# Kernel optimization log

Measured on AMD Instinct MI355X. Metric: run time of the kernel, lower is better.

## Reference

```python
import jax, jax.numpy as jnp
import numpy as np

N, NQ, NV, NE = 4, 256, 512, 256


def setup_inputs() -> dict:
    key = jax.random.key(0)
    ks = jax.random.split(key, 6)
    scale = 1.0 / np.sqrt(NE)
    return {
        "query": jax.random.normal(ks[0], (N, NQ, NE), dtype=jnp.float32),
        "context": jax.random.normal(ks[1], (N, NV, NE), dtype=jnp.float32),
        "memory": jax.random.normal(ks[2], (N, NV, NE), dtype=jnp.float32),
        "w_logit": jax.random.normal(ks[3], (NE,), dtype=jnp.float32) * scale,
        "b_logit": jnp.zeros((), dtype=jnp.float32),
        "temp": jnp.ones((), dtype=jnp.float32),
        "w_reduce": jax.random.normal(ks[4], (NE, NE), dtype=jnp.float32) * scale,
        "b_reduce": jnp.zeros((NE,), dtype=jnp.float32),
    }


def reference(query, context, memory, w_logit, b_logit, temp, w_reduce, b_reduce):
    # Additive (Bahdanau) attention, single-head branch of the torch module.
    # qc: [N, nQ, nV, nE] -- the large broadcast-add + tanh intermediate
    qc = jnp.tanh(query[:, :, None, :] + context[:, None, :, :])
    # fc_logit: Linear(nE -> 1), squeeze last dim -> [N, nQ, nV]
    logits = jnp.einsum("nqve,e->nqv", qc, w_logit) + b_logit
    probs = jax.nn.softmax(logits / temp, axis=2)
    # bmm(probs, memory) -> [N, nQ, nE], then leaky_relu (torch default slope 0.01)
    heads = jax.nn.leaky_relu(jnp.einsum("nqv,nve->nqe", probs, memory), negative_slope=0.01)
    # fc_reduceheads: Linear(nE -> nE), torch semantics y = x @ W.T + b
    return heads @ w_reduce.T + b_reduce
```

## Files before the change

kernel.cpp:

```cpp
#include <hip/hip_runtime.h>
#include <math.h>

#define N_B   4
#define NQ_   256
#define NV_   512
#define NE_   256

#define QSCALE 2.8853900817779268f

__device__ __forceinline__ float wave_reduce_sum(float v) {
#pragma unroll
    for (int m = 32; m > 0; m >>= 1) v += __shfl_xor(v, m, 64);
    return v;
}

__global__ __launch_bounds__(256) void prep_kernel(const float* __restrict__ C,
                                                   const float* __restrict__ W,
                                                   float* __restrict__ CT,
                                                   float* __restrict__ WT) {
    __shared__ float tile[64][65];
    const int b = blockIdx.x;
    const int col = threadIdx.x & 63, row4 = threadIdx.x >> 6;
    if (b < 128) {
        const int n  = b >> 5;
        const int e0 = ((b >> 3) & 3) * 64;
        const int v0 = (b & 7) * 64;
        const float* src = C + ((size_t)n * NV_ + v0) * NE_ + e0;
#pragma unroll
        for (int r = 0; r < 16; ++r) {
            const int vl = row4 + r * 4;
            tile[vl][col] = src[(size_t)vl * NE_ + col] * QSCALE;
        }
        __syncthreads();
        float* dst = CT + ((size_t)n * NE_ + e0) * NV_ + v0;
#pragma unroll
        for (int r = 0; r < 16; ++r) {
            const int el = row4 + r * 4;
            dst[(size_t)el * NV_ + col] = tile[col][el];
        }
    } else {
        const int bb = b - 128;
        const int r0 = (bb >> 2) * 64, c0 = (bb & 3) * 64;
        const float* src = W + (size_t)r0 * NE_ + c0;
#pragma unroll
        for (int r = 0; r < 16; ++r) {
            const int rl = row4 + r * 4;
            tile[rl][col] = src[(size_t)rl * NE_ + col];
        }
        __syncthreads();
        float* dst = WT + (size_t)c0 * NE_ + r0;
#pragma unroll
        for (int r = 0; r < 16; ++r) {
            const int cl = row4 + r * 4;
            dst[(size_t)cl * NE_ + col] = tile[col][cl];
        }
    }
}

#define QTA 4
__global__ __launch_bounds__(256, 8) void logits_kernel(
    const float* __restrict__ Q,
    const float* __restrict__ CT,
    const float* __restrict__ WL,
    float* __restrict__ S)
{
    const int n  = blockIdx.z;
    const int q0 = blockIdx.y * QTA;
    const int v0 = blockIdx.x * 64;
    const int tid = threadIdx.x;
    const int wv = tid >> 6, ln = tid & 63;

    __shared__ __align__(16) float s_q[NE_][QTA];
    __shared__ float s_w[NE_];
    __shared__ float s_part[4][QTA][64];

    {
        const int e = tid;
        s_w[e] = WL[e];
#pragma unroll
        for (int j = 0; j < QTA; ++j)
            s_q[e][j] = Q[((size_t)n * NQ_ + q0 + j) * NE_ + e] * QSCALE;
    }
    __syncthreads();

    const float* ct = CT + (size_t)n * NE_ * NV_ + v0 + ln;
    float acc0 = 0.f, acc1 = 0.f, acc2 = 0.f, acc3 = 0.f;
    const int e0 = wv * 64;
#pragma unroll 4
    for (int e = e0; e < e0 + 64; ++e) {
        const float c = ct[(size_t)e * NV_];
        const float4 q4 = *(const float4*)s_q[e];
        const float w = s_w[e];
        acc0 = fmaf(w, __builtin_amdgcn_rcpf(1.0f + __builtin_amdgcn_exp2f(c + q4.x)), acc0);
        acc1 = fmaf(w, __builtin_amdgcn_rcpf(1.0f + __builtin_amdgcn_exp2f(c + q4.y)), acc1);
        acc2 = fmaf(w, __builtin_amdgcn_rcpf(1.0f + __builtin_amdgcn_exp2f(c + q4.z)), acc2);
        acc3 = fmaf(w, __builtin_amdgcn_rcpf(1.0f + __builtin_amdgcn_exp2f(c + q4.w)), acc3);
    }
    s_part[wv][0][ln] = acc0;
    s_part[wv][1][ln] = acc1;
    s_part[wv][2][ln] = acc2;
    s_part[wv][3][ln] = acc3;
    __syncthreads();

    {
        const int j = tid >> 6, l = tid & 63;
        const float s = s_part[0][j][l] + s_part[1][j][l]
                      + s_part[2][j][l] + s_part[3][j][l];
        S[((size_t)n * NQ_ + q0 + j) * NV_ + v0 + l] = s;
    }
}

#define QTB 4
#define NWB 8
__global__ __launch_bounds__(512) void attn_out(
    const float* __restrict__ S,
    const float* __restrict__ M,
    const float* __restrict__ TEMP,
    const float* __restrict__ WRT,
    const float* __restrict__ BR,
    float* __restrict__ OUT)
{
    const int n  = blockIdx.y;
    const int q0 = blockIdx.x * QTB;
    const int tid = threadIdx.x;
    const int wv = tid >> 6, ln = tid & 63;

    __shared__ __align__(16) float s_prob[QTB][NV_];
    __shared__ __align__(16) float s_part[NWB][QTB][NE_];
    __shared__ __align__(16) float s_heads[QTB][NE_];

    if (wv < QTB) {
        const float scale = -2.0f / TEMP[0];
        const float* srow = S + ((size_t)n * NQ_ + q0 + wv) * NV_;
        float l[NV_ / 64];
        float mx = -1e30f;
#pragma unroll
        for (int k = 0; k < NV_ / 64; ++k) {
            l[k] = srow[ln + 64 * k] * scale;
            mx = fmaxf(mx, l[k]);
        }
#pragma unroll
        for (int m = 32; m > 0; m >>= 1) mx = fmaxf(mx, __shfl_xor(mx, m, 64));
        float sum = 0.0f;
#pragma unroll
        for (int k = 0; k < NV_ / 64; ++k) {
            l[k] = __expf(l[k] - mx);
            sum += l[k];
        }
        sum = wave_reduce_sum(sum);
        const float inv = 1.0f / sum;
#pragma unroll
        for (int k = 0; k < NV_ / 64; ++k) s_prob[wv][ln + 64 * k] = l[k] * inv;
    }
    __syncthreads();

    {
        const float4* M4 = (const float4*)(M + (size_t)n * NV_ * NE_);
        float4 h[QTB];
#pragma unroll
        for (int t = 0; t < QTB; ++t) h[t] = make_float4(0.f, 0.f, 0.f, 0.f);
        const int v0 = wv * (NV_ / NWB);
#pragma unroll 2
        for (int v = v0; v < v0 + NV_ / NWB; ++v) {
            const float4 m = M4[v * (NE_ / 4) + ln];
#pragma unroll
            for (int t = 0; t < QTB; ++t) {
                const float p = s_prob[t][v];
                h[t].x = fmaf(p, m.x, h[t].x);
                h[t].y = fmaf(p, m.y, h[t].y);
                h[t].z = fmaf(p, m.z, h[t].z);
                h[t].w = fmaf(p, m.w, h[t].w);
            }
        }
#pragma unroll
        for (int t = 0; t < QTB; ++t) ((float4*)s_part[wv][t])[ln] = h[t];
    }
    __syncthreads();

#pragma unroll
    for (int i = tid; i < QTB * NE_; i += 512) {
        const int t = i >> 8, e = i & (NE_ - 1);
        float s = 0.0f;
#pragma unroll
        for (int w = 0; w < NWB; ++w) s += s_part[w][t][e];
        s_heads[t][e] = (s > 0.0f) ? s : 0.01f * s;
    }
    __syncthreads();

    {
        const int t0 = (tid >> 8) * 2;
        const int ep = tid & 255;
        const float* w = WRT + ep;
        float a0 = 0.f, a1 = 0.f;
#pragma unroll 8
        for (int e = 0; e < NE_; ++e) {
            const float wv_ = w[(size_t)e * NE_];
            a0 = fmaf(s_heads[t0][e], wv_, a0);
            a1 = fmaf(s_heads[t0 + 1][e], wv_, a1);
        }
        const float b = BR[ep];
        OUT[((size_t)n * NQ_ + q0 + t0) * NE_ + ep]     = a0 + b;
        OUT[((size_t)n * NQ_ + q0 + t0 + 1) * NE_ + ep] = a1 + b;
    }
}

extern "C" void kernel_launch(void* const* d_in, const int* in_sizes, int n_in,
                              void* d_out, int out_size, void* d_ws, size_t ws_size,
                              hipStream_t stream) {
    const float* Q  = (const float*)d_in[0];
    const float* C  = (const float*)d_in[1];
    const float* M  = (const float*)d_in[2];
    const float* WL = (const float*)d_in[3];
    const float* T  = (const float*)d_in[5];
    const float* WR = (const float*)d_in[6];
    const float* BR = (const float*)d_in[7];
    float* OUT = (float*)d_out;

    float* CT  = (float*)d_ws;
    float* WRT = CT + (size_t)N_B * NE_ * NV_;
    float* S   = WRT + (size_t)NE_ * NE_;

    prep_kernel<<<dim3(128 + 16), 256, 0, stream>>>(C, WR, CT, WRT);

    dim3 ga(NV_ / 64, NQ_ / QTA, N_B);
    logits_kernel<<<ga, 256, 0, stream>>>(Q, CT, WL, S);

    dim3 gb(NQ_ / QTB, N_B);
    attn_out<<<gb, 512, 0, stream>>>(S, M, T, WRT, BR, OUT);
}
```

Before: 122.6 us.

## Factor exp of query plus context and pair terms to share one reciprocal

Context and query are pre-exponentiated, so exp2(c+q) becomes a product and the inner loop runs with no transcendental calls. Pairs of e terms are merged into one fraction (w0/a + w1/b = (w1*a + w0*b)/(a*b)), which halves the number of reciprocals. The aim is to offload the transcendental unit in the logits kernel, which is its bottleneck. In exchange, exponentiating separately can overflow or underflow for large inputs (exp2 of about 2.885*x) and the product a*b can overflow, so accuracy suffers at extreme values.

```diff
diff --git a/kernel.cpp b/kernel.cpp
--- a/kernel.cpp
+++ b/kernel.cpp
@@ -16,7 +16,7 @@
 
 __global__ __launch_bounds__(256) void prep_kernel(const float* __restrict__ C,
                                                    const float* __restrict__ W,
-                                                   float* __restrict__ CT,
+                                                   float* __restrict__ EC,
                                                    float* __restrict__ WT) {
     __shared__ float tile[64][65];
     const int b = blockIdx.x;
@@ -29,10 +29,10 @@
 #pragma unroll
         for (int r = 0; r < 16; ++r) {
             const int vl = row4 + r * 4;
-            tile[vl][col] = src[(size_t)vl * NE_ + col] * QSCALE;
+            tile[vl][col] = __builtin_amdgcn_exp2f(src[(size_t)vl * NE_ + col] * QSCALE);
         }
         __syncthreads();
-        float* dst = CT + ((size_t)n * NE_ + e0) * NV_ + v0;
+        float* dst = EC + ((size_t)n * NE_ + e0) * NV_ + v0;
 #pragma unroll
         for (int r = 0; r < 16; ++r) {
             const int el = row4 + r * 4;
@@ -60,7 +60,7 @@
 #define QTA 4
 __global__ __launch_bounds__(256, 8) void logits_kernel(
     const float* __restrict__ Q,
-    const float* __restrict__ CT,
+    const float* __restrict__ EC,
     const float* __restrict__ WL,
     float* __restrict__ S)
 {
@@ -79,22 +79,45 @@
         s_w[e] = WL[e];
 #pragma unroll
         for (int j = 0; j < QTA; ++j)
-            s_q[e][j] = Q[((size_t)n * NQ_ + q0 + j) * NE_ + e] * QSCALE;
-    }
-    __syncthreads();
-
-    const float* ct = CT + (size_t)n * NE_ * NV_ + v0 + ln;
+            s_q[e][j] = __builtin_amdgcn_exp2f(
+                Q[((size_t)n * NQ_ + q0 + j) * NE_ + e] * QSCALE);
+    }
+    __syncthreads();
+
+    const float* ec = EC + (size_t)n * NE_ * NV_ + v0 + ln;
     float acc0 = 0.f, acc1 = 0.f, acc2 = 0.f, acc3 = 0.f;
     const int e0 = wv * 64;
 #pragma unroll 4
-    for (int e = e0; e < e0 + 64; ++e) {
-        const float c = ct[(size_t)e * NV_];
-        const float4 q4 = *(const float4*)s_q[e];
-        const float w = s_w[e];
-        acc0 = fmaf(w, __builtin_amdgcn_rcpf(1.0f + __builtin_amdgcn_exp2f(c + q4.x)), acc0);
-        acc1 = fmaf(w, __builtin_amdgcn_rcpf(1.0f + __builtin_amdgcn_exp2f(c + q4.y)), acc1);
-        acc2 = fmaf(w, __builtin_amdgcn_rcpf(1.0f + __builtin_amdgcn_exp2f(c + q4.z)), acc2);
-        acc3 = fmaf(w, __builtin_amdgcn_rcpf(1.0f + __builtin_amdgcn_exp2f(c + q4.w)), acc3);
+    for (int e = e0; e < e0 + 64; e += 2) {
+        const float c0 = ec[(size_t)e * NV_];
+        const float c1 = ec[(size_t)(e + 1) * NV_];
+        const float4 qa = *(const float4*)s_q[e];
+        const float4 qb = *(const float4*)s_q[e + 1];
+        const float w0 = s_w[e], w1 = s_w[e + 1];
+        {
+            const float a = fmaf(c0, qa.x, 1.0f);
+            const float b = fmaf(c1, qb.x, 1.0f);
+            const float num = fmaf(w1, a, w0 * b);
+            acc0 = fmaf(num, __builtin_amdgcn_rcpf(a * b), acc0);
+        }
+        {
+            const float a = fmaf(c0, qa.y, 1.0f);
+            const float b = fmaf(c1, qb.y, 1.0f);
+            const float num = fmaf(w1, a, w0 * b);
+            acc1 = fmaf(num, __builtin_amdgcn_rcpf(a * b), acc1);
+        }
+        {
+            const float a = fmaf(c0, qa.z, 1.0f);
+            const float b = fmaf(c1, qb.z, 1.0f);
+            const float num = fmaf(w1, a, w0 * b);
+            acc2 = fmaf(num, __builtin_amdgcn_rcpf(a * b), acc2);
+        }
+        {
+            const float a = fmaf(c0, qa.w, 1.0f);
+            const float b = fmaf(c1, qb.w, 1.0f);
+            const float num = fmaf(w1, a, w0 * b);
+            acc3 = fmaf(num, __builtin_amdgcn_rcpf(a * b), acc3);
+        }
     }
     s_part[wv][0][ln] = acc0;
     s_part[wv][1][ln] = acc1;
@@ -216,14 +239,14 @@
     const float* BR = (const float*)d_in[7];
     float* OUT = (float*)d_out;
 
-    float* CT  = (float*)d_ws;
-    float* WRT = CT + (size_t)N_B * NE_ * NV_;
+    float* EC  = (float*)d_ws;
+    float* WRT = EC + (size_t)N_B * NE_ * NV_;
     float* S   = WRT + (size_t)NE_ * NE_;
 
-    prep_kernel<<<dim3(128 + 16), 256, 0, stream>>>(C, WR, CT, WRT);
+    prep_kernel<<<dim3(144), 256, 0, stream>>>(C, WR, EC, WRT);
 
     dim3 ga(NV_ / 64, NQ_ / QTA, N_B);
-    logits_kernel<<<ga, 256, 0, stream>>>(Q, CT, WL, S);
+    logits_kernel<<<ga, 256, 0, stream>>>(Q, EC, WL, S);
 
     dim3 gb(NQ_ / QTB, N_B);
     attn_out<<<gb, 512, 0, stream>>>(S, M, T, WRT, BR, OUT);
```

After: 108.9 us, median of 2. 1.13x faster.
